# Performance work log

Measured on AMD Instinct MI355X. Metric: run time of the kernel, lower is better.

Reference implementation:

```python
import jax, jax.numpy as jnp
import numpy as np

B, S, H, L, NH, FF, V = 32, 128, 768, 12, 12, 3072, 30522
D = H // NH


def _ln(x, s, b, eps=1e-12):
    mu = jnp.mean(x, -1, keepdims=True)
    var = jnp.mean((x - mu) ** 2, -1, keepdims=True)
    return s * (x - mu) * jax.lax.rsqrt(var + eps) + b


def setup_inputs() -> dict:
    key = jax.random.key(0)
    ks = jax.random.split(key, 16)
    n = lambda i, shape: 0.02 * jax.random.normal(ks[i], shape, jnp.float32)
    return {
        "fol_bert_indices": jax.random.randint(ks[0], (B, S), 0, V),
        "fol_bert_type": jnp.zeros((B, S), jnp.int32),
        "fol_bert_mask": jnp.ones((B, S), jnp.int32),
        "prompt_label_idx": jax.random.randint(ks[1], (1, 3), 0, V),
        # embeddings
        "word_emb": n(2, (V, H)),
        "pos_emb": n(3, (S, H)),
        "type_emb": n(4, (2, H)),
        "emb_ln_s": jnp.ones((H,), jnp.float32),
        "emb_ln_b": jnp.zeros((H,), jnp.float32),
        # stacked transformer layer params [L, ...]
        "Wq": n(5, (L, H, H)), "bq": jnp.zeros((L, H), jnp.float32),
        "Wk": n(6, (L, H, H)), "bk": jnp.zeros((L, H), jnp.float32),
        "Wv": n(7, (L, H, H)), "bv": jnp.zeros((L, H), jnp.float32),
        "Wo": n(8, (L, H, H)), "bo": jnp.zeros((L, H), jnp.float32),
        "ln1_s": jnp.ones((L, H), jnp.float32), "ln1_b": jnp.zeros((L, H), jnp.float32),
        "W1": n(9, (L, H, FF)), "b1": jnp.zeros((L, FF), jnp.float32),
        "W2": n(10, (L, FF, H)), "b2": jnp.zeros((L, H), jnp.float32),
        "ln2_s": jnp.ones((L, H), jnp.float32), "ln2_b": jnp.zeros((L, H), jnp.float32),
        # dense2 head (with_text=False branch)
        "d2_W": n(11, (H, H)), "d2_b": jnp.zeros((H,), jnp.float32),
    }


def reference(fol_bert_indices, fol_bert_type, fol_bert_mask, prompt_label_idx,
              word_emb, pos_emb, type_emb, emb_ln_s, emb_ln_b,
              Wq, bq, Wk, bk, Wv, bv, Wo, bo, ln1_s, ln1_b,
              W1, b1, W2, b2, ln2_s, ln2_b, d2_W, d2_b):
    # --- BERT embeddings ---
    x = word_emb[fol_bert_indices] + pos_emb[None, :, :] + type_emb[fol_bert_type]
    x = _ln(x, emb_ln_s, emb_ln_b)
    bias = (1.0 - fol_bert_mask.astype(jnp.float32))[:, None, None, :] * -1e9  # [B,1,1,S]
    inv_sqrt_d = 1.0 / float(D) ** 0.5

    def layer(h, p):
        wq, bq_, wk, bk_, wv, bv_, wo, bo_, s1, sb1, w1, fb1, w2, fb2, s2, sb2 = p
        q = (h @ wq + bq_).reshape(B, S, NH, D)
        k = (h @ wk + bk_).reshape(B, S, NH, D)
        v = (h @ wv + bv_).reshape(B, S, NH, D)
        att = jax.nn.softmax(jnp.einsum('bqhd,bkhd->bhqk', q, k) * inv_sqrt_d + bias, axis=-1)
        ctx = jnp.einsum('bhqk,bkhd->bqhd', att, v).reshape(B, S, H)
        h = _ln(h + ctx @ wo + bo_, s1, sb1)
        ff = jax.nn.gelu(h @ w1 + fb1) @ w2 + fb2
        return _ln(h + ff, s2, sb2), None

    x, _ = jax.lax.scan(layer, x, (Wq, bq, Wk, bk, Wv, bv, Wo, bo,
                                   ln1_s, ln1_b, W1, b1, W2, b2, ln2_s, ln2_b))

    # --- vectorized evaluate_expression over the batch ---
    # modeled as masked mean pooling of token hidden states over valid tokens
    valid = (fol_bert_indices != 0).astype(x.dtype)[..., None]  # [B,S,1]
    pooled = (x * valid).sum(1) / jnp.maximum(valid.sum(1), 1.0)  # [B,H]

    # with_text=False branch: dropout (identity in eval) + dense2
    out = pooled @ d2_W + d2_b  # [B,H]

    # label-word logits: out @ word_emb[prompt_label_idx[0]].T
    logits = out @ word_emb[prompt_label_idx[0]].T  # [B, 3]
    return logits
```

## Files before the change

kernel.cpp:

```cpp
#include <hip/hip_runtime.h>
#include <hip/hip_bf16.h>
#include <math.h>

typedef __bf16 v8bf __attribute__((ext_vector_type(8)));
typedef float v4f __attribute__((ext_vector_type(4)));

static constexpr int Bz = 32, Sq = 128, Hd = 768, Lr = 12, NHd = 12, FFd = 3072;
static constexpr int TOK = Bz * Sq;
static constexpr int QKVN = 3 * Hd;

__device__ __forceinline__ void gload16(const void* g, void* lds) {
  void* gg = const_cast<void*>(g);
  __builtin_amdgcn_global_load_lds(
      (__attribute__((address_space(1))) void*)gg,
      (__attribute__((address_space(3))) void*)lds, 16, 0, 0);
}

__device__ __forceinline__ float gelu_f(float x) {
  float u = 0.7978845608028654f * (x + 0.044715f * x * x * x);
  u = fminf(fmaxf(u, -15.f), 15.f);
  float e = __expf(2.f * u);
  return 0.5f * x * (1.f + (e - 1.f) / (e + 1.f));
}

__global__ __launch_bounds__(256) void transpose_cast(
    const float* __restrict__ in, __bf16* __restrict__ out, int K, int N,
    size_t in_zs, size_t out_zs) {
  const float* ib = in + (size_t)blockIdx.z * in_zs;
  __bf16* ob = out + (size_t)blockIdx.z * out_zs;
  __shared__ float tile[32][33];
  const int n0 = blockIdx.x * 32, k0 = blockIdx.y * 32;
  const int tx = threadIdx.x & 31, ty = threadIdx.x >> 5;
#pragma unroll
  for (int i = 0; i < 32; i += 8) tile[ty + i][tx] = ib[(size_t)(k0 + ty + i) * N + n0 + tx];
  __syncthreads();
#pragma unroll
  for (int i = 0; i < 32; i += 8) ob[(size_t)(n0 + ty + i) * K + k0 + tx] = (__bf16)tile[tx][ty + i];
}

__global__ __launch_bounds__(256) void concat_bias(
    const float* __restrict__ bq, const float* __restrict__ bk,
    const float* __restrict__ bv, float* __restrict__ bqkv) {
  const int i = blockIdx.x * 256 + threadIdx.x;
  if (i >= Lr * QKVN) return;
  const int l = i / QKVN, j = i % QKVN;
  float v = (j < Hd) ? bq[l * Hd + j] : (j < 2 * Hd) ? bk[l * Hd + j - Hd] : bv[l * Hd + j - 2 * Hd];
  bqkv[i] = v;
}

__device__ __forceinline__ void ln_write(float v0, float v1, float v2,
    const float* __restrict__ gs, const float* __restrict__ gb,
    float* __restrict__ xf, __bf16* __restrict__ xb, int t) {
  float sum = v0 + v1 + v2;
  float sq = v0 * v0 + v1 * v1 + v2 * v2;
#pragma unroll
  for (int o = 32; o > 0; o >>= 1) { sum += __shfl_xor(sum, o); sq += __shfl_xor(sq, o); }
  __shared__ float red[8];
  const int w = t >> 6;
  if ((t & 63) == 0) { red[w] = sum; red[4 + w] = sq; }
  __syncthreads();
  sum = red[0] + red[1] + red[2] + red[3];
  sq = red[4] + red[5] + red[6] + red[7];
  const float mu = sum * (1.f / 768.f);
  const float rs = rsqrtf(sq * (1.f / 768.f) - mu * mu + 1e-12f);
  float v[3] = {v0, v1, v2};
#pragma unroll
  for (int i = 0; i < 3; i++) {
    const int c = t + 256 * i;
    const float o = gs[c] * (v[i] - mu) * rs + gb[c];
    xf[c] = o;
    xb[c] = (__bf16)o;
  }
}

__global__ __launch_bounds__(256) void embed_ln(
    const int* __restrict__ idx, const int* __restrict__ typ,
    const float* __restrict__ we, const float* __restrict__ pe, const float* __restrict__ te,
    const float* __restrict__ gs, const float* __restrict__ gb,
    float* __restrict__ xf, __bf16* __restrict__ xb) {
  const int r = blockIdx.x, t = threadIdx.x;
  const int s = r & (Sq - 1);
  const size_t wrow = (size_t)idx[r] * Hd;
  const size_t trow = (size_t)typ[r] * Hd;
  float v[3];
#pragma unroll
  for (int i = 0; i < 3; i++) {
    const int c = t + 256 * i;
    v[i] = we[wrow + c] + pe[(size_t)s * Hd + c] + te[trow + c];
  }
  ln_write(v[0], v[1], v[2], gs, gb, xf + (size_t)r * Hd, xb + (size_t)r * Hd, t);
}

__global__ __launch_bounds__(256) void ln_k(
    const float* __restrict__ y0, const float* __restrict__ y1,
    const float* __restrict__ resid,
    const float* __restrict__ gs, const float* __restrict__ gb,
    float* __restrict__ xf, __bf16* __restrict__ xb) {
  const int r = blockIdx.x, t = threadIdx.x;
  float v[3];
#pragma unroll
  for (int i = 0; i < 3; i++) {
    const size_t o = (size_t)r * Hd + t + 256 * i;
    v[i] = y0[o] + y1[o] + resid[o];
  }
  ln_write(v[0], v[1], v[2], gs, gb, xf + (size_t)r * Hd, xb + (size_t)r * Hd, t);
}

template <int MODE>
__global__ __launch_bounds__(256) void gemm_bt(
    const __bf16* __restrict__ A, int lda, const __bf16* __restrict__ Bt, int ldb,
    const float* __restrict__ bias, void* __restrict__ C0, void* __restrict__ C1,
    int M, int N, int Klen) {
  __shared__ alignas(16) __bf16 As[128 * 32];
  __shared__ alignas(16) __bf16 Bs[128 * 32];
  const int z = blockIdx.z;
  A += (size_t)z * Klen;
  Bt += (size_t)z * Klen;
  void* Cout = (z == 0) ? C0 : C1;
  const int t = threadIdx.x;
  const int lane = t & 63, wave = t >> 6;
  const int wm = wave & 1, wn = wave >> 1;
  const int m0 = blockIdx.y * 128, n0 = blockIdx.x * 128;
  const v4f vzero = {0.f, 0.f, 0.f, 0.f};
  v4f acc[4][4];
#pragma unroll
  for (int i = 0; i < 4; i++)
#pragma unroll
    for (int j = 0; j < 4; j++) acc[i][j] = vzero;

  const int rA = t >> 2;
  const int kg = ((t & 3) - rA) & 3;
  const __bf16* Ag0 = A + (size_t)(m0 + rA) * lda + kg * 8;
  const __bf16* Ag1 = Ag0 + (size_t)64 * lda;
  const __bf16* Bg0 = Bt + (size_t)(n0 + rA) * ldb + kg * 8;
  const __bf16* Bg1 = Bg0 + (size_t)64 * ldb;
  char* AsL = (char*)As + wave * 1024;
  char* BsL = (char*)Bs + wave * 1024;
  const int cn = lane & 15, q = lane >> 4;
  const int kiter = Klen >> 5;
  for (int kt = 0; kt < kiter; ++kt) {
    __syncthreads();
    gload16(Ag0, AsL);
    gload16(Ag1, AsL + 4096);
    gload16(Bg0, BsL);
    gload16(Bg1, BsL + 4096);
    Ag0 += 32; Ag1 += 32; Bg0 += 32; Bg1 += 32;
    __syncthreads();
    v8bf a[4], b[4];
#pragma unroll
    for (int i = 0; i < 4; i++) {
      const int ra = wm * 64 + i * 16 + cn;
      a[i] = *(const v8bf*)&As[ra * 32 + ((q + ra) & 3) * 8];
      const int rb = wn * 64 + i * 16 + cn;
      b[i] = *(const v8bf*)&Bs[rb * 32 + ((q + rb) & 3) * 8];
    }
#pragma unroll
    for (int i = 0; i < 4; i++)
#pragma unroll
      for (int j = 0; j < 4; j++)
        acc[i][j] = __builtin_amdgcn_mfma_f32_16x16x32_bf16(a[i], b[j], acc[i][j], 0, 0, 0);
  }
#pragma unroll
  for (int i = 0; i < 4; i++) {
    const int row0 = m0 + wm * 64 + i * 16 + q * 4;
#pragma unroll
    for (int j = 0; j < 4; j++) {
      const int col = n0 + wn * 64 + j * 16 + cn;
      const float bv = (MODE == 3) ? ((z == 0) ? bias[col] : 0.f) : bias[col];
#pragma unroll
      for (int r = 0; r < 4; r++) {
        const size_t off = (size_t)(row0 + r) * N + col;
        float v = acc[i][j][r] + bv;
        if (MODE == 0) {
          ((__bf16*)Cout)[off] = (__bf16)v;
        } else if (MODE == 3) {
          ((float*)Cout)[off] = v;
        } else {
          ((__bf16*)Cout)[off] = (__bf16)gelu_f(v);
        }
      }
    }
  }
}

__global__ __launch_bounds__(256) void attn_k(
    const __bf16* __restrict__ qkv, const int* __restrict__ mask, __bf16* __restrict__ ctx) {
  const int bh = blockIdx.x;
  const int b = bh / NHd, h = bh % NHd;
  union SmemU {
    struct { __bf16 Q[128][72]; __bf16 K[128][72]; } qk;
    __bf16 P[128][136];
  };
  __shared__ alignas(16) SmemU u;
  __shared__ alignas(16) __bf16 Vt[64][136];
  __shared__ float biasS[128];
  const int t = threadIdx.x, lane = t & 63, w = t >> 6;
  const int cn = lane & 15, q = lane >> 4;
  const __bf16* base = qkv + (size_t)b * Sq * QKVN + h * 64;
  for (int i = t; i < 1024; i += 256) {
    const int r = i >> 3, c = (i & 7) << 3;
    *(uint4*)&u.qk.Q[r][c] = *(const uint4*)(base + (size_t)r * QKVN + c);
    *(uint4*)&u.qk.K[r][c] = *(const uint4*)(base + (size_t)r * QKVN + Hd + c);
    union { uint4 u4; ushort us[8]; } tv;
    tv.u4 = *(const uint4*)(base + (size_t)r * QKVN + 2 * Hd + c);
#pragma unroll
    for (int j = 0; j < 8; j++) Vt[c + j][r] = ((const __bf16*)tv.us)[j];
  }
  if (t < 128) biasS[t] = (1.f - (float)mask[b * Sq + t]) * -1e9f;
  __syncthreads();

  const v4f vzero = {0.f, 0.f, 0.f, 0.f};
  v4f sc[2][8];
#pragma unroll
  for (int i = 0; i < 2; i++)
#pragma unroll
    for (int j = 0; j < 8; j++) sc[i][j] = vzero;
#pragma unroll
  for (int ks = 0; ks < 2; ks++) {
    v8bf a0 = *(const v8bf*)&u.qk.Q[32 * w + cn][ks * 32 + q * 8];
    v8bf a1 = *(const v8bf*)&u.qk.Q[32 * w + 16 + cn][ks * 32 + q * 8];
#pragma unroll
    for (int nt = 0; nt < 8; nt++) {
      v8bf bk = *(const v8bf*)&u.qk.K[16 * nt + cn][ks * 32 + q * 8];
      sc[0][nt] = __builtin_amdgcn_mfma_f32_16x16x32_bf16(a0, bk, sc[0][nt], 0, 0, 0);
      sc[1][nt] = __builtin_amdgcn_mfma_f32_16x16x32_bf16(a1, bk, sc[1][nt], 0, 0, 0);
    }
  }
#pragma unroll
  for (int mt = 0; mt < 2; mt++)
#pragma unroll
    for (int rg = 0; rg < 4; rg++) {
      float vv[8];
      float mx = -3.0e38f;
#pragma unroll
      for (int nt = 0; nt < 8; nt++) {
        vv[nt] = sc[mt][nt][rg] * 0.125f + biasS[16 * nt + cn];
        mx = fmaxf(mx, vv[nt]);
      }
#pragma unroll
      for (int o = 1; o < 16; o <<= 1) mx = fmaxf(mx, __shfl_xor(mx, o));
      float sum = 0.f;
#pragma unroll
      for (int nt = 0; nt < 8; nt++) { vv[nt] = __expf(vv[nt] - mx); sum += vv[nt]; }
#pragma unroll
      for (int o = 1; o < 16; o <<= 1) sum += __shfl_xor(sum, o);
      const float inv = 1.f / sum;
#pragma unroll
      for (int nt = 0; nt < 8; nt++) sc[mt][nt][rg] = vv[nt] * inv;
    }
  __syncthreads();
#pragma unroll
  for (int mt = 0; mt < 2; mt++)
#pragma unroll
    for (int nt = 0; nt < 8; nt++)
#pragma unroll
      for (int rg = 0; rg < 4; rg++)
        u.P[32 * w + 16 * mt + q * 4 + rg][16 * nt + cn] = (__bf16)sc[mt][nt][rg];
  __syncthreads();
  v4f oc[2][4];
#pragma unroll
  for (int i = 0; i < 2; i++)
#pragma unroll
    for (int j = 0; j < 4; j++) oc[i][j] = vzero;
#pragma unroll
  for (int ks = 0; ks < 4; ks++) {
    v8bf a0 = *(const v8bf*)&u.P[32 * w + cn][ks * 32 + q * 8];
    v8bf a1 = *(const v8bf*)&u.P[32 * w + 16 + cn][ks * 32 + q * 8];
#pragma unroll
    for (int nt = 0; nt < 4; nt++) {
      v8bf bv = *(const v8bf*)&Vt[16 * nt + cn][ks * 32 + q * 8];
      oc[0][nt] = __builtin_amdgcn_mfma_f32_16x16x32_bf16(a0, bv, oc[0][nt], 0, 0, 0);
      oc[1][nt] = __builtin_amdgcn_mfma_f32_16x16x32_bf16(a1, bv, oc[1][nt], 0, 0, 0);
    }
  }
  __bf16* cb = ctx + (size_t)b * Sq * Hd + h * 64;
#pragma unroll
  for (int mt = 0; mt < 2; mt++)
#pragma unroll
    for (int nt = 0; nt < 4; nt++)
#pragma unroll
      for (int rg = 0; rg < 4; rg++)
        cb[(size_t)(32 * w + 16 * mt + q * 4 + rg) * Hd + 16 * nt + cn] = (__bf16)oc[mt][nt][rg];
}

__global__ __launch_bounds__(256) void headw_k(
    const float* __restrict__ d2W, const float* __restrict__ d2b,
    const int* __restrict__ lab, const float* __restrict__ we,
    float* __restrict__ u, float* __restrict__ s) {
  const int t = threadIdx.x, w = t >> 6, k = blockIdx.x;
  __shared__ float red[12];
  if (k < 768) {
    float dv[3];
#pragma unroll
    for (int i = 0; i < 3; i++) dv[i] = d2W[(size_t)k * 768 + t + 256 * i];
    float acc[3];
#pragma unroll
    for (int c = 0; c < 3; c++) {
      const float* wr = we + (size_t)lab[c] * 768;
      float a = 0.f;
#pragma unroll
      for (int i = 0; i < 3; i++) a += dv[i] * wr[t + 256 * i];
#pragma unroll
      for (int o = 32; o > 0; o >>= 1) a += __shfl_xor(a, o);
      acc[c] = a;
    }
    if ((t & 63) == 0) {
#pragma unroll
      for (int c = 0; c < 3; c++) red[c * 4 + w] = acc[c];
    }
    __syncthreads();
    if (t < 3) u[t * 768 + k] = red[t * 4] + red[t * 4 + 1] + red[t * 4 + 2] + red[t * 4 + 3];
  } else {
    const int c = k - 768;
    const float* wr = we + (size_t)lab[c] * 768;
    float a = 0.f;
#pragma unroll
    for (int i = 0; i < 3; i++) a += d2b[t + 256 * i] * wr[t + 256 * i];
#pragma unroll
    for (int o = 32; o > 0; o >>= 1) a += __shfl_xor(a, o);
    if ((t & 63) == 0) red[w] = a;
    __syncthreads();
    if (t == 0) s[c] = red[0] + red[1] + red[2] + red[3];
  }
}

__global__ __launch_bounds__(256) void pool_logits(
    const float* __restrict__ xf, const int* __restrict__ idx,
    const float* __restrict__ u, const float* __restrict__ s,
    float* __restrict__ out) {
  const int b = blockIdx.x, t = threadIdx.x, w = t >> 6;
  __shared__ float validS[128];
  __shared__ float pooled[768];
  __shared__ float red[12];
  if (t < 128) validS[t] = (idx[b * 128 + t] != 0) ? 1.f : 0.f;
  __syncthreads();
  float cnt = 0.f;
  for (int s2 = 0; s2 < 128; s2++) cnt += validS[s2];
  const float icnt = 1.f / fmaxf(cnt, 1.f);
#pragma unroll
  for (int i = 0; i < 3; i++) {
    const int c = t + 256 * i;
    float acc = 0.f;
    for (int s2 = 0; s2 < 128; s2++) acc += xf[(size_t)(b * 128 + s2) * 768 + c] * validS[s2];
    pooled[c] = acc * icnt;
  }
  __syncthreads();
  for (int c = 0; c < 3; c++) {
    float p = 0.f;
    for (int j = t; j < 768; j += 256) p += pooled[j] * u[c * 768 + j];
#pragma unroll
    for (int o = 32; o > 0; o >>= 1) p += __shfl_xor(p, o);
    if ((t & 63) == 0) red[c * 4 + w] = p;
  }
  __syncthreads();
  if (t < 3) out[b * 3 + t] = red[t * 4] + red[t * 4 + 1] + red[t * 4 + 2] + red[t * 4 + 3] + s[t];
}

extern "C" void kernel_launch(void* const* d_in, const int* in_sizes, int n_in,
                              void* d_out, int out_size, void* d_ws, size_t ws_size,
                              hipStream_t stream) {
  const int* idx = (const int*)d_in[0];
  const int* typ = (const int*)d_in[1];
  const int* msk = (const int*)d_in[2];
  const int* lab = (const int*)d_in[3];
  const float* we = (const float*)d_in[4];
  const float* pe = (const float*)d_in[5];
  const float* te = (const float*)d_in[6];
  const float* elns = (const float*)d_in[7];
  const float* elnb = (const float*)d_in[8];
  const float* Wq = (const float*)d_in[9];
  const float* bq = (const float*)d_in[10];
  const float* Wk = (const float*)d_in[11];
  const float* bk = (const float*)d_in[12];
  const float* Wv = (const float*)d_in[13];
  const float* bv = (const float*)d_in[14];
  const float* Wo = (const float*)d_in[15];
  const float* bo = (const float*)d_in[16];
  const float* l1s = (const float*)d_in[17];
  const float* l1b = (const float*)d_in[18];
  const float* W1 = (const float*)d_in[19];
  const float* b1 = (const float*)d_in[20];
  const float* W2 = (const float*)d_in[21];
  const float* b2 = (const float*)d_in[22];
  const float* l2s = (const float*)d_in[23];
  const float* l2b = (const float*)d_in[24];
  const float* d2W = (const float*)d_in[25];
  const float* d2b = (const float*)d_in[26];

  char* p = (char*)d_ws;
  auto carve = [&](size_t bytes) { char* r = p; p += (bytes + 255) & ~(size_t)255; return r; };
  __bf16* Wqkvt = (__bf16*)carve((size_t)Lr * QKVN * Hd * 2);
  __bf16* Wot   = (__bf16*)carve((size_t)Lr * Hd * Hd * 2);
  __bf16* W1t   = (__bf16*)carve((size_t)Lr * FFd * Hd * 2);
  __bf16* W2t   = (__bf16*)carve((size_t)Lr * Hd * FFd * 2);
  float*  bqkv  = (float*)carve((size_t)Lr * QKVN * 4);
  float*  xf    = (float*)carve((size_t)TOK * Hd * 4);
  __bf16* xb    = (__bf16*)carve((size_t)TOK * Hd * 2);
  __bf16* qkvB  = (__bf16*)carve((size_t)TOK * QKVN * 2);
  __bf16* ctxB  = (__bf16*)carve((size_t)TOK * Hd * 2);
  float*  yf    = (float*)carve((size_t)TOK * Hd * 4);
  __bf16* gB    = (__bf16*)carve((size_t)TOK * FFd * 2);
  float*  uB    = (float*)carve(3 * 768 * 4);
  float*  sB    = (float*)carve(4 * 4);
  float*  yf2   = (float*)qkvB;

  dim3 blk(256);
  transpose_cast<<<dim3(24, 24, 12), blk, 0, stream>>>(Wq, Wqkvt, Hd, Hd, (size_t)Hd * Hd, (size_t)QKVN * Hd);
  transpose_cast<<<dim3(24, 24, 12), blk, 0, stream>>>(Wk, Wqkvt + (size_t)Hd * Hd, Hd, Hd, (size_t)Hd * Hd, (size_t)QKVN * Hd);
  transpose_cast<<<dim3(24, 24, 12), blk, 0, stream>>>(Wv, Wqkvt + (size_t)2 * Hd * Hd, Hd, Hd, (size_t)Hd * Hd, (size_t)QKVN * Hd);
  transpose_cast<<<dim3(24, 24, 12), blk, 0, stream>>>(Wo, Wot, Hd, Hd, (size_t)Hd * Hd, (size_t)Hd * Hd);
  transpose_cast<<<dim3(96, 24, 12), blk, 0, stream>>>(W1, W1t, Hd, FFd, (size_t)Hd * FFd, (size_t)FFd * Hd);
  transpose_cast<<<dim3(24, 96, 12), blk, 0, stream>>>(W2, W2t, FFd, Hd, (size_t)FFd * Hd, (size_t)Hd * FFd);
  concat_bias<<<dim3((Lr * QKVN + 255) / 256), blk, 0, stream>>>(bq, bk, bv, bqkv);
  headw_k<<<dim3(771), blk, 0, stream>>>(d2W, d2b, lab, we, uB, sB);

  embed_ln<<<dim3(TOK), blk, 0, stream>>>(idx, typ, we, pe, te, elns, elnb, xf, xb);

  for (int l = 0; l < Lr; l++) {
    gemm_bt<0><<<dim3(QKVN / 128, TOK / 128, 1), blk, 0, stream>>>(
        xb, Hd, Wqkvt + (size_t)l * QKVN * Hd, Hd, bqkv + l * QKVN, qkvB, nullptr, TOK, QKVN, Hd);
    attn_k<<<dim3(Bz * NHd), blk, 0, stream>>>(qkvB, msk, ctxB);
    gemm_bt<3><<<dim3(Hd / 128, TOK / 128, 2), blk, 0, stream>>>(
        ctxB, Hd, Wot + (size_t)l * Hd * Hd, Hd, bo + l * Hd, yf, yf2, TOK, Hd, Hd / 2);
    ln_k<<<dim3(TOK), blk, 0, stream>>>(yf, yf2, xf, l1s + l * Hd, l1b + l * Hd, xf, xb);
    gemm_bt<2><<<dim3(FFd / 128, TOK / 128, 1), blk, 0, stream>>>(
        xb, Hd, W1t + (size_t)l * FFd * Hd, Hd, b1 + l * FFd, gB, nullptr, TOK, FFd, Hd);
    gemm_bt<3><<<dim3(Hd / 128, TOK / 128, 2), blk, 0, stream>>>(
        gB, FFd, W2t + (size_t)l * Hd * FFd, FFd, b2 + l * Hd, yf, yf2, TOK, Hd, FFd / 2);
    ln_k<<<dim3(TOK), blk, 0, stream>>>(yf, yf2, xf, l2s + l * Hd, l2b + l * Hd, xf, xb);
  }

  pool_logits<<<dim3(Bz), blk, 0, stream>>>(xf, idx, uB, sB, (float*)d_out);
}
```

Before: 2.607 ms.

## Double GEMM K-tile to 64 and swizzle workgroup order across XCDs

The bf16 GEMM kernel now stages a 64-wide K slice per iteration instead of 32, which halves the number of barrier pairs and loads per unit of work and issues two MFMA k-steps per staged tile. The LDS swizzle is widened from 4 to 8 chunk groups to match. A workgroup index remap groups blocks in strides of eight so that neighbouring tiles land on the same XCD and share L2. The cost is doubled LDS per block, which may lower occupancy, and there is still no double buffering.

```diff
diff --git a/kernel.cpp b/kernel.cpp
--- a/kernel.cpp
+++ b/kernel.cpp
@@ -111,8 +111,8 @@
     const __bf16* __restrict__ A, int lda, const __bf16* __restrict__ Bt, int ldb,
     const float* __restrict__ bias, void* __restrict__ C0, void* __restrict__ C1,
     int M, int N, int Klen) {
-  __shared__ alignas(16) __bf16 As[128 * 32];
-  __shared__ alignas(16) __bf16 Bs[128 * 32];
+  __shared__ alignas(16) __bf16 As[128 * 64];
+  __shared__ alignas(16) __bf16 Bs[128 * 64];
   const int z = blockIdx.z;
   A += (size_t)z * Klen;
   Bt += (size_t)z * Klen;
@@ -120,7 +120,14 @@
   const int t = threadIdx.x;
   const int lane = t & 63, wave = t >> 6;
   const int wm = wave & 1, wn = wave >> 1;
-  const int m0 = blockIdx.y * 128, n0 = blockIdx.x * 128;
+
+  const int nwg = gridDim.x * gridDim.y;
+  int orig = blockIdx.y * gridDim.x + blockIdx.x;
+  int swz = orig;
+  if ((nwg & 7) == 0) swz = (orig & 7) * (nwg >> 3) + (orig >> 3);
+  const int bx = swz % gridDim.x, by = swz / gridDim.x;
+  const int m0 = by * 128, n0 = bx * 128;
+
   const v4f vzero = {0.f, 0.f, 0.f, 0.f};
   v4f acc[4][4];
 #pragma unroll
@@ -128,37 +135,39 @@
 #pragma unroll
     for (int j = 0; j < 4; j++) acc[i][j] = vzero;
 
-  const int rA = t >> 2;
-  const int kg = ((t & 3) - rA) & 3;
-  const __bf16* Ag0 = A + (size_t)(m0 + rA) * lda + kg * 8;
-  const __bf16* Ag1 = Ag0 + (size_t)64 * lda;
-  const __bf16* Bg0 = Bt + (size_t)(n0 + rA) * ldb + kg * 8;
-  const __bf16* Bg1 = Bg0 + (size_t)64 * ldb;
+  const int rA = t >> 3;
+  const int kg = ((t & 7) - rA) & 7;
+  const __bf16* Ag = A + (size_t)(m0 + rA) * lda + kg * 8;
+  const __bf16* Bg = Bt + (size_t)(n0 + rA) * ldb + kg * 8;
   char* AsL = (char*)As + wave * 1024;
   char* BsL = (char*)Bs + wave * 1024;
   const int cn = lane & 15, q = lane >> 4;
-  const int kiter = Klen >> 5;
+  const int kiter = Klen >> 6;
   for (int kt = 0; kt < kiter; ++kt) {
     __syncthreads();
-    gload16(Ag0, AsL);
-    gload16(Ag1, AsL + 4096);
-    gload16(Bg0, BsL);
-    gload16(Bg1, BsL + 4096);
-    Ag0 += 32; Ag1 += 32; Bg0 += 32; Bg1 += 32;
+#pragma unroll
+    for (int i = 0; i < 4; i++) {
+      gload16(Ag + (size_t)(32 * i) * lda, AsL + 4096 * i);
+      gload16(Bg + (size_t)(32 * i) * ldb, BsL + 4096 * i);
+    }
+    Ag += 64; Bg += 64;
     __syncthreads();
-    v8bf a[4], b[4];
-#pragma unroll
-    for (int i = 0; i < 4; i++) {
-      const int ra = wm * 64 + i * 16 + cn;
-      a[i] = *(const v8bf*)&As[ra * 32 + ((q + ra) & 3) * 8];
-      const int rb = wn * 64 + i * 16 + cn;
-      b[i] = *(const v8bf*)&Bs[rb * 32 + ((q + rb) & 3) * 8];
-    }
-#pragma unroll
-    for (int i = 0; i < 4; i++)
-#pragma unroll
-      for (int j = 0; j < 4; j++)
-        acc[i][j] = __builtin_amdgcn_mfma_f32_16x16x32_bf16(a[i], b[j], acc[i][j], 0, 0, 0);
+#pragma unroll
+    for (int kk = 0; kk < 2; kk++) {
+      v8bf a[4], b[4];
+#pragma unroll
+      for (int i = 0; i < 4; i++) {
+        const int ra = wm * 64 + i * 16 + cn;
+        a[i] = *(const v8bf*)&As[ra * 64 + (((kk << 2) + q + ra) & 7) * 8];
+        const int rb = wn * 64 + i * 16 + cn;
+        b[i] = *(const v8bf*)&Bs[rb * 64 + (((kk << 2) + q + rb) & 7) * 8];
+      }
+#pragma unroll
+      for (int i = 0; i < 4; i++)
+#pragma unroll
+        for (int j = 0; j < 4; j++)
+          acc[i][j] = __builtin_amdgcn_mfma_f32_16x16x32_bf16(a[i], b[j], acc[i][j], 0, 0, 0);
+    }
   }
 #pragma unroll
   for (int i = 0; i < 4; i++) {
```

New measurement: 2.372 ms. 1.1x faster.
